# Performance work log

Measured on AMD Instinct MI355X. Metric: run time of the kernel, lower is better.

## Reference

```python
import jax, jax.numpy as jnp
import numpy as np

B, Q, H, W = 64, 300, 40, 40  # batch, num_queries, feature-map H,W (img/32)


def setup_inputs() -> dict:
    key = jax.random.key(0)
    k1, k2, k3 = jax.random.split(key, 3)
    obj_coord = jax.random.uniform(k1, (B, Q, 4), dtype=jnp.float32)  # sigmoid cxcywh
    sub_coord = jax.random.uniform(k2, (B, Q, 4), dtype=jnp.float32)
    img_size = jax.random.randint(k3, (B, 2), 800, 1280, dtype=jnp.int64)  # (h, w)
    mask = jnp.zeros((B, H, W), dtype=bool)  # only its shape is used
    return {"obj_coord": obj_coord, "sub_coord": sub_coord, "img_size": img_size, "mask": mask}


def _box_cxcywh_to_xyxy(b):
    cx, cy, w, h = b[..., 0], b[..., 1], b[..., 2], b[..., 3]
    return cx - 0.5 * w, cy - 0.5 * h, cx + 0.5 * w, cy + 0.5 * h


def _mask_from_query(coord, img_size, Hm, Wm):
    # coord: [B,Q,4] cxcywh in [0,1]; img_size: [B,2] = (img_h, img_w)
    x1, y1, x2, y2 = _box_cxcywh_to_xyxy(coord)
    sw = img_size[:, 1:2].astype(jnp.float32)  # [B,1]
    sh = img_size[:, 0:1].astype(jnp.float32)
    # torch: (coord * size) // 32 then .long()  (floor division on floats == floor)
    x1 = jnp.floor(x1 * sw / 32.0).astype(jnp.int32)
    y1 = jnp.floor(y1 * sh / 32.0).astype(jnp.int32)
    x2 = jnp.floor(x2 * sw / 32.0).astype(jnp.int32)
    y2 = jnp.floor(y2 * sh / 32.0).astype(jnp.int32)
    x2 = jnp.minimum(x2, Wm - 1)
    y2 = jnp.minimum(y2, Hm - 1)
    hh = jnp.arange(Hm, dtype=jnp.int32)[:, None]  # [H,1]
    ww = jnp.arange(Wm, dtype=jnp.int32)[None, :]  # [1,W]
    # True OUTSIDE the (inclusive) box: single fused broadcast compare, [B,Q,H,W]
    return ((hh < y1[..., None, None]) | (hh > y2[..., None, None]) |
            (ww < x1[..., None, None]) | (ww > x2[..., None, None]))


def reference(obj_coord, sub_coord, img_size, mask):
    Hm, Wm = mask.shape[1], mask.shape[2]
    mask_object = _mask_from_query(obj_coord, img_size, Hm, Wm)
    mask_human = _mask_from_query(sub_coord, img_size, Hm, Wm)
    # stack object/human masks; float32 so fwd and fwdbwd share output structure
    return jnp.stack([mask_object, mask_human], axis=0).astype(jnp.float32)
```

## Files before the change

kernel.cpp:

```cpp
#include <hip/hip_runtime.h>
#include <stdint.h>


#define B_   64
#define Q_   300
#define HM   40
#define WM   40
#define NBOX 38400
#define EPW  4

__global__ __launch_bounds__(256) void partmap_fused(
    const float* __restrict__ obj,
    const float* __restrict__ sub,
    const int*   __restrict__ img,
    float4*      __restrict__ out)
{
    #pragma clang fp contract(off)
    const int tid  = threadIdx.x;
    const int lane = tid & 63;
    const int wid  = (blockIdx.x << 2) | (tid >> 6);
    const int e0   = wid * EPW;

    int h_j[7], sh_j[7];
    #pragma unroll
    for (int j = 0; j < 7; ++j) {
        int p  = j * 64 + lane;
        int h  = p / 10;
        int w4 = p - 10 * h;
        h_j[j]  = h;
        sh_j[j] = w4 * 4;
    }

    int id = e0 + (lane & 3);
    int q  = id % Q_;
    int sb = id / Q_;
    int b  = sb & 63;
    int s  = sb >> 6;

    const float* coord = s ? sub : obj;
    float4 c = ((const float4*)coord)[b * Q_ + q];

    float shh = (float)img[b * 2 + 0];
    float sww = (float)img[b * 2 + 1];

    float x1f = (c.x - 0.5f * c.z) * sww / 32.0f;
    float y1f = (c.y - 0.5f * c.w) * shh / 32.0f;
    float x2f = (c.x + 0.5f * c.z) * sww / 32.0f;
    float y2f = (c.y + 0.5f * c.w) * shh / 32.0f;

    int x1 = (int)floorf(x1f);
    int y1 = (int)floorf(y1f);
    int x2 = min((int)floorf(x2f), WM - 1);
    int y2 = min((int)floorf(y2f), HM - 1);

    uint64_t blo = (x1 <= 0) ? ~0ull : ~((1ull << x1) - 1ull);
    uint64_t bhi = (1ull << (x2 + 1)) - 1ull;
    uint64_t outside = (~(blo & bhi)) & ((1ull << 40) - 1ull);
    uint32_t d0 = (uint32_t)outside;
    uint32_t d1 = (uint32_t)(outside >> 32);

    float4* bp = out + (size_t)e0 * 400 + lane;

    #pragma unroll
    for (int e = 0; e < EPW; ++e) {
        uint32_t sd0 = (uint32_t)__builtin_amdgcn_readlane((int)d0, e);
        uint32_t sd1 = (uint32_t)__builtin_amdgcn_readlane((int)d1, e);
        int      sy1 = __builtin_amdgcn_readlane(y1, e);
        int      sy2 = __builtin_amdgcn_readlane(y2, e);
        uint64_t m64 = ((uint64_t)sd1 << 32) | (uint64_t)sd0;
        float4*  ep  = bp + e * 400;

        #pragma unroll
        for (int j = 0; j < 7; ++j) {
            int rneg = ((h_j[j] - sy1) | (sy2 - h_j[j])) >> 31;
            uint32_t m = (uint32_t)(m64 >> sh_j[j]) | (uint32_t)rneg;
            float4 r;
            r.x = (float)( m        & 1u);
            r.y = (float)((m >> 1u) & 1u);
            r.z = (float)((m >> 2u) & 1u);
            r.w = (float)((m >> 3u) & 1u);
            if (j < 6 || lane < 16)
                ep[j * 64] = r;
        }
    }
}

extern "C" void kernel_launch(void* const* d_in, const int* in_sizes, int n_in,
                              void* d_out, int out_size, void* d_ws, size_t ws_size,
                              hipStream_t stream) {
    const float* obj = (const float*)d_in[0];
    const float* sub = (const float*)d_in[1];
    const int*   img = (const int*)d_in[2];

    float4* out = (float4*)d_out;

    partmap_fused<<<dim3(NBOX / (EPW * 4)), dim3(256), 0, stream>>>(obj, sub, img, out);
}
```

Measured before the change: 240.6 us.

## Use fixed-size grid with per-wave box loop instead of one-shot waves

```diff
diff --git a/kernel.cpp b/kernel.cpp
--- a/kernel.cpp
+++ b/kernel.cpp
@@ -7,78 +7,71 @@
 #define HM   40
 #define WM   40
 #define NBOX 38400
-#define EPW  4
 
-__global__ __launch_bounds__(256) void partmap_fused(
+typedef float f4_native __attribute__((ext_vector_type(4)));
+
+__global__ __launch_bounds__(256) void partmap_persist(
     const float* __restrict__ obj,
     const float* __restrict__ sub,
     const int*   __restrict__ img,
-    float4*      __restrict__ out)
+    f4_native*   __restrict__ out)
 {
     #pragma clang fp contract(off)
-    const int tid  = threadIdx.x;
-    const int lane = tid & 63;
-    const int wid  = (blockIdx.x << 2) | (tid >> 6);
-    const int e0   = wid * EPW;
+    const int lane = threadIdx.x & 63;
+    const int w    = (blockIdx.x << 2) | (threadIdx.x >> 6);
+
+    const int e0 = (w * 75) >> 4;
+    const int e1 = ((w + 1) * 75) >> 4;
 
     int h_j[7], sh_j[7];
     #pragma unroll
     for (int j = 0; j < 7; ++j) {
         int p  = j * 64 + lane;
-        int h  = p / 10;
+        int h  = (int)((unsigned)p / 10u);
         int w4 = p - 10 * h;
         h_j[j]  = h;
         sh_j[j] = w4 * 4;
     }
 
-    int id = e0 + (lane & 3);
-    int q  = id % Q_;
-    int sb = id / Q_;
-    int b  = sb & 63;
-    int s  = sb >> 6;
+    for (int e = e0; e < e1; ++e) {
+        int q  = e % Q_;
+        int sb = e / Q_;
+        int b  = sb & 63;
+        int s  = sb >> 6;
 
-    const float* coord = s ? sub : obj;
-    float4 c = ((const float4*)coord)[b * Q_ + q];
+        const float* coord = s ? sub : obj;
+        float4 c = ((const float4*)coord)[b * Q_ + q];
 
-    float shh = (float)img[b * 2 + 0];
-    float sww = (float)img[b * 2 + 1];
+        float shh = (float)img[b * 2 + 0];
+        float sww = (float)img[b * 2 + 1];
 
-    float x1f = (c.x - 0.5f * c.z) * sww / 32.0f;
-    float y1f = (c.y - 0.5f * c.w) * shh / 32.0f;
-    float x2f = (c.x + 0.5f * c.z) * sww / 32.0f;
-    float y2f = (c.y + 0.5f * c.w) * shh / 32.0f;
+        float x1f = (c.x - 0.5f * c.z) * sww / 32.0f;
+        float y1f = (c.y - 0.5f * c.w) * shh / 32.0f;
+        float x2f = (c.x + 0.5f * c.z) * sww / 32.0f;
+        float y2f = (c.y + 0.5f * c.w) * shh / 32.0f;
 
-    int x1 = (int)floorf(x1f);
-    int y1 = (int)floorf(y1f);
-    int x2 = min((int)floorf(x2f), WM - 1);
-    int y2 = min((int)floorf(y2f), HM - 1);
+        int x1 = (int)floorf(x1f);
+        int y1 = (int)floorf(y1f);
+        int x2 = min((int)floorf(x2f), WM - 1);
+        int y2 = min((int)floorf(y2f), HM - 1);
 
-    uint64_t blo = (x1 <= 0) ? ~0ull : ~((1ull << x1) - 1ull);
-    uint64_t bhi = (1ull << (x2 + 1)) - 1ull;
-    uint64_t outside = (~(blo & bhi)) & ((1ull << 40) - 1ull);
-    uint32_t d0 = (uint32_t)outside;
-    uint32_t d1 = (uint32_t)(outside >> 32);
+        uint64_t blo = (x1 <= 0) ? ~0ull : ~((1ull << x1) - 1ull);
+        uint64_t bhi = (1ull << (x2 + 1)) - 1ull;
+        uint64_t outside = (~(blo & bhi)) & ((1ull << 40) - 1ull);
 
-    float4* bp = out + (size_t)e0 * 400 + lane;
-
-    #pragma unroll
-    for (int e = 0; e < EPW; ++e) {
-        uint32_t sd0 = (uint32_t)__builtin_amdgcn_readlane((int)d0, e);
-        uint32_t sd1 = (uint32_t)__builtin_amdgcn_readlane((int)d1, e);
-        int      sy1 = __builtin_amdgcn_readlane(y1, e);
-        int      sy2 = __builtin_amdgcn_readlane(y2, e);
-        uint64_t m64 = ((uint64_t)sd1 << 32) | (uint64_t)sd0;
-        float4*  ep  = bp + e * 400;
+        f4_native* ep = out + (size_t)e * 400 + lane;
 
         #pragma unroll
         for (int j = 0; j < 7; ++j) {
-            int rneg = ((h_j[j] - sy1) | (sy2 - h_j[j])) >> 31;
-            uint32_t m = (uint32_t)(m64 >> sh_j[j]) | (uint32_t)rneg;
-            float4 r;
+            int rneg = ((h_j[j] - y1) | (y2 - h_j[j])) >> 31;
+            uint32_t m = (uint32_t)(outside >> sh_j[j]) | (uint32_t)rneg;
+
+            f4_native r;
             r.x = (float)( m        & 1u);
             r.y = (float)((m >> 1u) & 1u);
             r.z = (float)((m >> 2u) & 1u);
             r.w = (float)((m >> 3u) & 1u);
+
             if (j < 6 || lane < 16)
                 ep[j * 64] = r;
         }
@@ -92,7 +85,7 @@
     const float* sub = (const float*)d_in[1];
     const int*   img = (const int*)d_in[2];
 
-    float4* out = (float4*)d_out;
+    f4_native* out = (f4_native*)d_out;
 
-    partmap_fused<<<dim3(NBOX / (EPW * 4)), dim3(256), 0, stream>>>(obj, sub, img, out);
+    partmap_persist<<<dim3(2048), dim3(256), 0, stream>>>(obj, sub, img, out);
 }
```

New measurement: 239.6 us. Within noise of the previous version (-0.4%).
